# Performance work log

Hardware: AMD Instinct MI355X
Metric: run time of the kernel (lower is better)

The kernel has to match this reference:

```python
import jax, jax.numpy as jnp
import numpy as np

B, K, D = 16384, 64, 128


def setup_inputs() -> dict:
    key = jax.random.key(0)
    kx, kc = jax.random.split(key)
    x = jax.random.normal(kx, (B, D), dtype=jnp.float32)
    centers = jax.random.uniform(kc, (K, D), dtype=jnp.float32)  # torch.rand init
    return {"x": x, "centers": centers}


def reference(x, centers):
    batch, dim = x.shape
    k = centers.shape[0]
    # pairwise squared distances, same math as sum((x - c)^2)
    diff = x[:, None, :] - centers[None, :, :]          # [B, K, D]
    dist_sq = jnp.sum(diff * diff, axis=-1)             # [B, K]
    expo = -0.5 * dist_sq
    # safe softmax over clusters (identical to max-subtracted exp/sum)
    resp = jax.nn.softmax(expo, axis=-1)                # [B, K]
    log_resp = jnp.log(jnp.clip(resp, 1e-8))
    # hard assignment and per-cluster statistics
    assign = jnp.argmin(dist_sq, axis=-1)               # [B] int
    onehot = jax.nn.one_hot(assign, k, dtype=x.dtype)   # [B, K]
    cluster_weight = jnp.sum(onehot, axis=0)            # [K]
    emp_total = jnp.einsum('nk,nd->kd', onehot, x)      # [K, D]
    emp_mean = emp_total / (cluster_weight[:, None] + 1e-7)
    # masked centered samples: onehot[n,k]*(x_n - mean_k) is nonzero only at k=assign(n)
    xm = x - emp_mean[assign]                           # [B, D]
    covar_total = jnp.einsum('nk,nd,ne->kde', onehot, xm, xm)  # [K, D, D]
    covar = covar_total / (cluster_weight[:, None, None] + 1e-7)
    eye = jnp.eye(dim, dtype=x.dtype)
    covar_diag = covar * eye
    covar_off = covar * (1.0 - eye)
    diag_dist_sq = jnp.sum((covar_diag - eye) ** 2, axis=(1, 2))  # [K]
    off_dist_sq = jnp.sum(covar_off ** 2, axis=(1, 2))            # [K]
    mean_dist_sq = jnp.sum((emp_mean - centers) ** 2, axis=1)     # [K]
    mean_mse = jnp.sum(cluster_weight * mean_dist_sq) / (batch * dim)
    covar_mse = jnp.sum(
        cluster_weight * diag_dist_sq / (batch * dim)
        + cluster_weight * off_dist_sq / (batch * dim * (dim - 1.0))
    )
    return log_resp, mean_mse, covar_mse
```

## Files before the change

kernel.cpp:

```cpp
#include <hip/hip_runtime.h>

#define BB 16384
#define KK 64
#define DD 128
#define SEG 256
#define MAXITEMS 128
#define RSLAB 4096
#define RBLKS 256

typedef __attribute__((ext_vector_type(8))) short bf16x8;
typedef __attribute__((ext_vector_type(4))) float f32x4;

__device__ __forceinline__ unsigned int packbf2(float a, float b) {
    unsigned ua = __float_as_uint(a);
    unsigned ub = __float_as_uint(b);
    ua = (ua + 0x7FFFu + ((ua >> 16) & 1u)) >> 16;
    ub = (ub + 0x7FFFu + ((ub >> 16) & 1u)) >> 16;
    return ua | (ub << 16);
}

__global__ __launch_bounds__(256) void k_rows(
    const float* __restrict__ x, const float* __restrict__ centers,
    float* __restrict__ log_resp, int* __restrict__ assign,
    int* __restrict__ bhist, int* __restrict__ counter)
{
    __shared__ float xs[64][132];
    __shared__ float ct[DD][66];
    __shared__ float cn2[KK];
    __shared__ int   lh[KK];

    const int tid = threadIdx.x;
    const int row0 = blockIdx.x * 64;

    if (blockIdx.x == 0 && tid == 0) *counter = 0;
    if (tid < KK) lh[tid] = 0;

    for (int g = tid; g < 64 * 32; g += 256) {
        int r = g >> 5, c4 = g & 31;
        float4 v = ((const float4*)(x + (size_t)(row0 + r) * DD))[c4];
        *(float4*)&xs[r][c4 * 4] = v;
    }
    for (int g = tid; g < KK * 32; g += 256) {
        int k = g >> 5, c4 = g & 31;
        float4 v = ((const float4*)(centers + (size_t)k * DD))[c4];
        ct[c4 * 4 + 0][k] = v.x;
        ct[c4 * 4 + 1][k] = v.y;
        ct[c4 * 4 + 2][k] = v.z;
        ct[c4 * 4 + 3][k] = v.w;
    }
    __syncthreads();
    if (tid < KK) {
        float s = 0.f;
        for (int d = 0; d < DD; ++d) { float c = ct[d][tid]; s = fmaf(c, c, s); }
        cn2[tid] = s;
    }
    __syncthreads();

    const int tr = tid >> 5;
    const int tc = tid & 31;
    const int k0 = tc * 2, k1 = k0 + 1;

    float acc0[8], acc1[8];
    #pragma unroll
    for (int i = 0; i < 8; ++i) { acc0[i] = 0.f; acc1[i] = 0.f; }

    for (int d = 0; d < DD; d += 4) {
        float2 b0 = *(const float2*)&ct[d + 0][k0];
        float2 b1 = *(const float2*)&ct[d + 1][k0];
        float2 b2 = *(const float2*)&ct[d + 2][k0];
        float2 b3 = *(const float2*)&ct[d + 3][k0];
        #pragma unroll
        for (int i = 0; i < 8; ++i) {
            float4 a = *(const float4*)&xs[tr * 8 + i][d];
            acc0[i] = fmaf(a.x, b0.x, acc0[i]);
            acc1[i] = fmaf(a.x, b0.y, acc1[i]);
            acc0[i] = fmaf(a.y, b1.x, acc0[i]);
            acc1[i] = fmaf(a.y, b1.y, acc1[i]);
            acc0[i] = fmaf(a.z, b2.x, acc0[i]);
            acc1[i] = fmaf(a.z, b2.y, acc1[i]);
            acc0[i] = fmaf(a.w, b3.x, acc0[i]);
            acc1[i] = fmaf(a.w, b3.y, acc1[i]);
        }
    }

    const float cn0 = 0.5f * cn2[k0], cn1 = 0.5f * cn2[k1];
    #pragma unroll
    for (int i = 0; i < 8; ++i) {
        int row = row0 + tr * 8 + i;
        float v0 = acc0[i] - cn0;
        float v1 = acc1[i] - cn1;
        float m; int idx;
        if (v1 > v0) { m = v1; idx = k1; } else { m = v0; idx = k0; }
        #pragma unroll
        for (int off = 1; off < 32; off <<= 1) {
            float ov = __shfl_xor(m, off);
            int   oi = __shfl_xor(idx, off);
            if (ov > m || (ov == m && oi < idx)) { m = ov; idx = oi; }
        }
        float s = expf(v0 - m) + expf(v1 - m);
        #pragma unroll
        for (int off = 1; off < 32; off <<= 1) s += __shfl_xor(s, off);
        float ls = logf(s);
        float lr0 = fmaxf(v0 - m - ls, -18.4206807f);
        float lr1 = fmaxf(v1 - m - ls, -18.4206807f);
        *(float2*)&log_resp[(size_t)row * KK + k0] = make_float2(lr0, lr1);
        if (tc == 0) {
            assign[row] = idx;
            atomicAdd(&lh[idx], 1);
        }
    }
    __syncthreads();
    if (tid < KK) bhist[blockIdx.x * KK + tid] = lh[tid];
}

__global__ __launch_bounds__(256) void k_seg2(
    const float* __restrict__ x, const int* __restrict__ assign,
    const int* __restrict__ bhist,
    float* __restrict__ part, float* __restrict__ emp_part)
{
    __shared__ int ph_tot[4][KK];
    __shared__ int cnt_s[KK];
    __shared__ int sc[2][256];
    __shared__ int pre_s[257];
    __shared__ int myk_s, myseg_s;
    __shared__ int rows_s[SEG];
    __shared__ unsigned int XT[DD][68];

    const int tid = threadIdx.x;
    const int b = blockIdx.x;
    const int w = tid >> 6, lane = tid & 63;

    {
        const int t = tid & 63, q = tid >> 6;
        int tot = 0;
        for (int bb = q * 64; bb < q * 64 + 64; ++bb)
            tot += bhist[bb * KK + t];
        ph_tot[q][t] = tot;
    }
    __syncthreads();
    if (tid < KK)
        cnt_s[tid] = ph_tot[0][tid] + ph_tot[1][tid] + ph_tot[2][tid] + ph_tot[3][tid];
    __syncthreads();
    if (tid == 0) {
        int ic = 0;
        myk_s = -1;
        for (int k = 0; k < KK; ++k) {
            int ns = (cnt_s[k] + SEG - 1) / SEG;
            if (b >= ic && b < ic + ns) { myk_s = k; myseg_s = b - ic; }
            ic += ns;
        }
    }
    __syncthreads();
    if (myk_s < 0) return;

    const int kC = myk_s;
    const int lo = myseg_s * SEG;
    const int hi = min(lo + SEG, cnt_s[kC]);
    const int len = hi - lo;

    {
        int v = bhist[tid * KK + kC];
        sc[0][tid] = v;
        __syncthreads();
        int buf = 0;
        #pragma unroll
        for (int off = 1; off < 256; off <<= 1) {
            int nv = sc[buf][tid];
            if (tid >= off) nv += sc[buf][tid - off];
            sc[buf ^ 1][tid] = nv;
            buf ^= 1;
            __syncthreads();
        }
        if (tid == 0) pre_s[0] = 0;
        pre_s[tid + 1] = sc[buf][tid];
    }
    __syncthreads();

    for (int g = w; g < 256; g += 4) {
        int p0 = pre_s[g], p1 = pre_s[g + 1];
        if (p1 <= lo || p0 >= hi) continue;
        int a = assign[g * 64 + lane];
        bool m = (a == kC);
        unsigned long long bal = __ballot(m);
        if (m) {
            int rank = __popcll(bal & ((1ull << lane) - 1ull));
            int pos = p0 + rank;
            if (pos >= lo && pos < hi) rows_s[pos - lo] = g * 64 + lane;
        }
    }
    __syncthreads();

    const int c4 = lane & 15, q = lane >> 4;
    f32x4 acc[2][8];
    #pragma unroll
    for (int h = 0; h < 2; ++h)
        #pragma unroll
        for (int nt = 0; nt < 8; ++nt)
            acc[h][nt] = (f32x4){0.f, 0.f, 0.f, 0.f};
    float colsum = 0.f;

    for (int half = 0; half < 2; ++half) {
        const int hoff = half * 128;
        const int hlen = min(128, len - hoff);
        if (hlen <= 0) break;

        __syncthreads();
        {
            const int r0 = 2 * lane, r1 = 2 * lane + 1;
            const int d0 = w * 32;
            const float* p0 = x + (size_t)rows_s[hoff + (r0 < hlen ? r0 : 0)] * DD + d0;
            const float* p1 = x + (size_t)rows_s[hoff + (r1 < hlen ? r1 : 0)] * DD + d0;
            #pragma unroll
            for (int i = 0; i < 8; ++i) {
                float4 a = make_float4(0.f, 0.f, 0.f, 0.f);
                float4 bb = make_float4(0.f, 0.f, 0.f, 0.f);
                if (r0 < hlen) a  = *(const float4*)(p0 + 4 * i);
                if (r1 < hlen) bb = *(const float4*)(p1 + 4 * i);
                XT[d0 + 4 * i + 0][lane] = packbf2(a.x, bb.x);
                XT[d0 + 4 * i + 1][lane] = packbf2(a.y, bb.y);
                XT[d0 + 4 * i + 2][lane] = packbf2(a.z, bb.z);
                XT[d0 + 4 * i + 3][lane] = packbf2(a.w, bb.w);
            }
        }
        __syncthreads();

        if (tid < DD) {
            float s = 0.f;
            #pragma unroll
            for (int j4 = 0; j4 < 16; ++j4) {
                uint4 v = *(const uint4*)&XT[tid][j4 * 4];
                s += __uint_as_float(v.x << 16) + __uint_as_float(v.x & 0xFFFF0000u);
                s += __uint_as_float(v.y << 16) + __uint_as_float(v.y & 0xFFFF0000u);
                s += __uint_as_float(v.z << 16) + __uint_as_float(v.z & 0xFFFF0000u);
                s += __uint_as_float(v.w << 16) + __uint_as_float(v.w & 0xFFFF0000u);
            }
            colsum += s;
        }

        #pragma unroll
        for (int c = 0; c < 4; ++c) {
            const int ku = c * 16 + q * 4;
            bf16x8 a0 = *(const bf16x8*)&XT[(2 * w + 0) * 16 + c4][ku];
            bf16x8 a1 = *(const bf16x8*)&XT[(2 * w + 1) * 16 + c4][ku];
            #pragma unroll
            for (int nt = 0; nt < 8; ++nt) {
                bf16x8 bb = *(const bf16x8*)&XT[nt * 16 + c4][ku];
                acc[0][nt] = __builtin_amdgcn_mfma_f32_16x16x32_bf16(a0, bb, acc[0][nt], 0, 0, 0);
                acc[1][nt] = __builtin_amdgcn_mfma_f32_16x16x32_bf16(a1, bb, acc[1][nt], 0, 0, 0);
            }
        }
    }

    if (tid < DD) emp_part[b * DD + tid] = colsum;

    float* pb = part + (size_t)b * (DD * DD);
    #pragma unroll
    for (int h = 0; h < 2; ++h) {
        const int m0 = (2 * w + h) * 16 + q * 4;
        #pragma unroll
        for (int nt = 0; nt < 8; ++nt) {
            const int n = nt * 16 + c4;
            pb[(m0 + 0) * DD + n] = acc[h][nt].x;
            pb[(m0 + 1) * DD + n] = acc[h][nt].y;
            pb[(m0 + 2) * DD + n] = acc[h][nt].z;
            pb[(m0 + 3) * DD + n] = acc[h][nt].w;
        }
    }
}

__global__ __launch_bounds__(256) void k_redfinal(
    const float* __restrict__ part, const float* __restrict__ emp_part,
    const int* __restrict__ bhist, const float* __restrict__ centers,
    float2* __restrict__ spart, int* __restrict__ counter,
    float* __restrict__ outscalars)
{
    __shared__ int ph_tot[4][KK];
    __shared__ int cnt_s[KK], ist_s[KK], ien_s[KK];
    __shared__ float mu_s[DD], emp_s[DD];
    __shared__ float emp2[2][DD];
    __shared__ float red[4][RSLAB];

    const int tid = threadIdx.x;
    const int b = blockIdx.x;
    const int kD = b >> 2, p = b & 3;
    const int w = tid >> 6, lane = tid & 63;

    {
        const int t = tid & 63, q = tid >> 6;
        int tot = 0;
        for (int bb = q * 64; bb < q * 64 + 64; ++bb)
            tot += bhist[bb * KK + t];
        ph_tot[q][t] = tot;
    }
    __syncthreads();
    if (tid < KK)
        cnt_s[tid] = ph_tot[0][tid] + ph_tot[1][tid] + ph_tot[2][tid] + ph_tot[3][tid];
    __syncthreads();
    if (tid == 0) {
        int ic = 0;
        for (int k = 0; k < KK; ++k) {
            ist_s[k] = ic;
            ic += (cnt_s[k] + SEG - 1) / SEG;
            ien_s[k] = ic;
        }
    }
    __syncthreads();

    const int i0 = ist_s[kD], i1 = ien_s[kD];
    const float wgt = (float)cnt_s[kD];
    const float inv = 1.0f / (wgt + 1e-7f);

    {
        const int dh = tid & 127, hf = tid >> 7;
        float e0 = 0.f, e1 = 0.f;
        int it = i0 + hf;
        for (; it + 2 < i1; it += 4) {
            e0 += emp_part[it * DD + dh];
            e1 += emp_part[(it + 2) * DD + dh];
        }
        if (it < i1) e0 += emp_part[it * DD + dh];
        emp2[hf][dh] = e0 + e1;
    }
    __syncthreads();
    if (tid < DD) {
        float e = emp2[0][tid] + emp2[1][tid];
        emp_s[tid] = e;
        mu_s[tid] = e * inv;
    }

    float4 acc[16];
    #pragma unroll
    for (int c = 0; c < 16; ++c) acc[c] = make_float4(0.f, 0.f, 0.f, 0.f);

    const int base = p * RSLAB;
    for (int it = i0 + w; it < i1; it += 4) {
        const float* pb = part + (size_t)it * (DD * DD) + base;
        #pragma unroll
        for (int c = 0; c < 16; ++c) {
            float4 v = *(const float4*)&pb[c * 256 + lane * 4];
            acc[c].x += v.x; acc[c].y += v.y; acc[c].z += v.z; acc[c].w += v.w;
        }
    }
    #pragma unroll
    for (int c = 0; c < 16; ++c)
        *(float4*)&red[w][c * 256 + lane * 4] = acc[c];
    __syncthreads();

    float ds = 0.f, os = 0.f, mm = 0.f;
    #pragma unroll
    for (int jj = 0; jj < 16; ++jj) {
        int el = jj * 256 + tid;
        float sx = red[0][el] + red[1][el] + red[2][el] + red[3][el];
        int gel = base + el;
        int d = gel >> 7, e = gel & 127;
        float ctv = sx - mu_s[d] * emp_s[e] - emp_s[d] * mu_s[e]
                  + wgt * mu_s[d] * mu_s[e];
        float v = ctv * inv;
        if (d == e) { float t = v - 1.f; ds += t * t; }
        else        { os += v * v; }
    }
    if (p == 0 && tid < DD) {
        float t = mu_s[tid] - centers[kD * DD + tid];
        mm = t * t;
    }

    #pragma unroll
    for (int off = 32; off > 0; off >>= 1) {
        ds += __shfl_down(ds, off);
        os += __shfl_down(os, off);
        mm += __shfl_down(mm, off);
    }
    __shared__ float rds[4], ros[4], rmm[4];
    __shared__ int is_last;
    if (lane == 0) { rds[w] = ds; ros[w] = os; rmm[w] = mm; }
    __syncthreads();
    if (tid == 0) {
        float DS = rds[0] + rds[1] + rds[2] + rds[3];
        float OS = ros[0] + ros[1] + ros[2] + ros[3];
        float MM = rmm[0] + rmm[1] + rmm[2] + rmm[3];
        const float bd = (float)BB * (float)DD;
        float2 mine;
        mine.x = wgt * MM / bd;
        mine.y = wgt * DS / bd + wgt * OS / (bd * (float)(DD - 1));
        spart[b] = mine;
        __threadfence();
        int old = atomicAdd(counter, 1);
        is_last = (old == RBLKS - 1);
    }
    __syncthreads();
    if (is_last) {
        __threadfence();
        float2 v = spart[tid];
        float a = v.x, bb = v.y;
        #pragma unroll
        for (int off = 32; off > 0; off >>= 1) {
            a  += __shfl_down(a, off);
            bb += __shfl_down(bb, off);
        }
        __shared__ float ra[4], rb[4];
        if (lane == 0) { ra[w] = a; rb[w] = bb; }
        __syncthreads();
        if (tid == 0) {
            outscalars[0] = ra[0] + ra[1] + ra[2] + ra[3];
            outscalars[1] = rb[0] + rb[1] + rb[2] + rb[3];
        }
    }
}

extern "C" void kernel_launch(void* const* d_in, const int* in_sizes, int n_in,
                              void* d_out, int out_size, void* d_ws, size_t ws_size,
                              hipStream_t stream) {
    const float* x = (const float*)d_in[0];
    const float* centers = (const float*)d_in[1];
    float* out = (float*)d_out;
    float* outscalars = out + (size_t)BB * KK;

    char* ws = (char*)d_ws;
    size_t off = 0;
    float*  part     = (float*)(ws + off); off += (size_t)MAXITEMS * DD * DD * 4;
    float*  emp_part = (float*)(ws + off); off += MAXITEMS * DD * 4;
    int*    assign   = (int*)  (ws + off); off += BB * 4;
    int*    bhist    = (int*)  (ws + off); off += 256 * KK * 4;
    float2* spart    = (float2*)(ws + off); off += RBLKS * 8;
    int*    counter  = (int*)  (ws + off); off += 256;

    k_rows    <<<256, 256, 0, stream>>>(x, centers, out, assign, bhist, counter);
    k_seg2    <<<MAXITEMS, 256, 0, stream>>>(x, assign, bhist, part, emp_part);
    k_redfinal<<<RBLKS, 256, 0, stream>>>(part, emp_part, bhist, centers,
                                          spart, counter, outscalars);
}
```

Before: 135.3 us.

## Shrink covariance segments to 64 rows and transpose block histogram layout

```diff
diff --git a/kernel.cpp b/kernel.cpp
--- a/kernel.cpp
+++ b/kernel.cpp
@@ -3,8 +3,9 @@
 #define BB 16384
 #define KK 64
 #define DD 128
-#define SEG 256
-#define MAXITEMS 128
+#define GRP 64
+#define NGRP 256
+#define MAXITEMS 320
 #define RSLAB 4096
 #define RBLKS 256
 
@@ -22,7 +23,7 @@
 __global__ __launch_bounds__(256) void k_rows(
     const float* __restrict__ x, const float* __restrict__ centers,
     float* __restrict__ log_resp, int* __restrict__ assign,
-    int* __restrict__ bhist, int* __restrict__ counter)
+    int* __restrict__ bhistT, int* __restrict__ counter)
 {
     __shared__ float xs[64][132];
     __shared__ float ct[DD][66];
@@ -110,12 +111,12 @@
         }
     }
     __syncthreads();
-    if (tid < KK) bhist[blockIdx.x * KK + tid] = lh[tid];
+    if (tid < KK) bhistT[tid * NGRP + blockIdx.x] = lh[tid];
 }
 
 __global__ __launch_bounds__(256) void k_seg2(
     const float* __restrict__ x, const int* __restrict__ assign,
-    const int* __restrict__ bhist,
+    const int* __restrict__ bhistT,
     float* __restrict__ part, float* __restrict__ emp_part)
 {
     __shared__ int ph_tot[4][KK];
@@ -123,19 +124,23 @@
     __shared__ int sc[2][256];
     __shared__ int pre_s[257];
     __shared__ int myk_s, myseg_s;
-    __shared__ int rows_s[SEG];
-    __shared__ unsigned int XT[DD][68];
+    __shared__ int rows_s[GRP];
+    __shared__ unsigned int XR[GRP][68];
+    __shared__ unsigned int XT[DD][36];
 
     const int tid = threadIdx.x;
     const int b = blockIdx.x;
     const int w = tid >> 6, lane = tid & 63;
 
     {
-        const int t = tid & 63, q = tid >> 6;
-        int tot = 0;
-        for (int bb = q * 64; bb < q * 64 + 64; ++bb)
-            tot += bhist[bb * KK + t];
-        ph_tot[q][t] = tot;
+        const int k = tid & 63, q = tid >> 6;
+        const int* p = bhistT + k * NGRP + q * 64;
+        int t0 = 0, t1 = 0, t2 = 0, t3 = 0;
+        #pragma unroll 4
+        for (int i = 0; i < 64; i += 4) {
+            t0 += p[i]; t1 += p[i + 1]; t2 += p[i + 2]; t3 += p[i + 3];
+        }
+        ph_tot[q][k] = t0 + t1 + t2 + t3;
     }
     __syncthreads();
     if (tid < KK)
@@ -145,7 +150,7 @@
         int ic = 0;
         myk_s = -1;
         for (int k = 0; k < KK; ++k) {
-            int ns = (cnt_s[k] + SEG - 1) / SEG;
+            int ns = (cnt_s[k] + GRP - 1) / GRP;
             if (b >= ic && b < ic + ns) { myk_s = k; myseg_s = b - ic; }
             ic += ns;
         }
@@ -154,12 +159,12 @@
     if (myk_s < 0) return;
 
     const int kC = myk_s;
-    const int lo = myseg_s * SEG;
-    const int hi = min(lo + SEG, cnt_s[kC]);
+    const int lo = myseg_s * GRP;
+    const int hi = min(lo + GRP, cnt_s[kC]);
     const int len = hi - lo;
 
     {
-        int v = bhist[tid * KK + kC];
+        int v = bhistT[kC * NGRP + tid];
         sc[0][tid] = v;
         __syncthreads();
         int buf = 0;
@@ -176,7 +181,7 @@
     }
     __syncthreads();
 
-    for (int g = w; g < 256; g += 4) {
+    for (int g = w; g < NGRP; g += 4) {
         int p0 = pre_s[g], p1 = pre_s[g + 1];
         if (p1 <= lo || p0 >= hi) continue;
         int a = assign[g * 64 + lane];
@@ -190,6 +195,57 @@
     }
     __syncthreads();
 
+    #pragma unroll
+    for (int sub = 0; sub < 4; ++sub) {
+        const int j = sub * 16 + (tid >> 4);
+        const int c8 = (tid & 15) * 8;
+        float4 a = make_float4(0.f, 0.f, 0.f, 0.f);
+        float4 c = make_float4(0.f, 0.f, 0.f, 0.f);
+        if (j < len) {
+            const float* p = x + (size_t)rows_s[j] * DD + c8;
+            a = *(const float4*)p;
+            c = *(const float4*)(p + 4);
+        }
+        uint4 pk;
+        pk.x = packbf2(a.x, a.y);
+        pk.y = packbf2(a.z, a.w);
+        pk.z = packbf2(c.x, c.y);
+        pk.w = packbf2(c.z, c.w);
+        *(uint4*)&XR[j][c8 >> 1] = pk;
+    }
+    __syncthreads();
+
+    {
+        const int rp = lane & 31;
+        const int d0 = w * 32 + (lane >> 5) * 16;
+        const int dp0 = d0 >> 1;
+        uint4 a0 = *(const uint4*)&XR[2 * rp][dp0];
+        uint4 a1 = *(const uint4*)&XR[2 * rp][dp0 + 4];
+        uint4 b0 = *(const uint4*)&XR[2 * rp + 1][dp0];
+        uint4 b1 = *(const uint4*)&XR[2 * rp + 1][dp0 + 4];
+        unsigned int A[8] = {a0.x, a0.y, a0.z, a0.w, a1.x, a1.y, a1.z, a1.w};
+        unsigned int B[8] = {b0.x, b0.y, b0.z, b0.w, b1.x, b1.y, b1.z, b1.w};
+        #pragma unroll
+        for (int i = 0; i < 8; ++i) {
+            XT[d0 + 2 * i + 0][rp] = (A[i] & 0xFFFFu) | (B[i] << 16);
+            XT[d0 + 2 * i + 1][rp] = (A[i] >> 16) | (B[i] & 0xFFFF0000u);
+        }
+    }
+    __syncthreads();
+
+    if (tid < DD) {
+        float s = 0.f;
+        #pragma unroll
+        for (int j4 = 0; j4 < 8; ++j4) {
+            uint4 v = *(const uint4*)&XT[tid][j4 * 4];
+            s += __uint_as_float(v.x << 16) + __uint_as_float(v.x & 0xFFFF0000u);
+            s += __uint_as_float(v.y << 16) + __uint_as_float(v.y & 0xFFFF0000u);
+            s += __uint_as_float(v.z << 16) + __uint_as_float(v.z & 0xFFFF0000u);
+            s += __uint_as_float(v.w << 16) + __uint_as_float(v.w & 0xFFFF0000u);
+        }
+        emp_part[b * DD + tid] = s;
+    }
+
     const int c4 = lane & 15, q = lane >> 4;
     f32x4 acc[2][8];
     #pragma unroll
@@ -197,61 +253,19 @@
         #pragma unroll
         for (int nt = 0; nt < 8; ++nt)
             acc[h][nt] = (f32x4){0.f, 0.f, 0.f, 0.f};
-    float colsum = 0.f;
-
-    for (int half = 0; half < 2; ++half) {
-        const int hoff = half * 128;
-        const int hlen = min(128, len - hoff);
-        if (hlen <= 0) break;
-
-        __syncthreads();
-        {
-            const int r0 = 2 * lane, r1 = 2 * lane + 1;
-            const int d0 = w * 32;
-            const float* p0 = x + (size_t)rows_s[hoff + (r0 < hlen ? r0 : 0)] * DD + d0;
-            const float* p1 = x + (size_t)rows_s[hoff + (r1 < hlen ? r1 : 0)] * DD + d0;
-            #pragma unroll
-            for (int i = 0; i < 8; ++i) {
-                float4 a = make_float4(0.f, 0.f, 0.f, 0.f);
-                float4 bb = make_float4(0.f, 0.f, 0.f, 0.f);
-                if (r0 < hlen) a  = *(const float4*)(p0 + 4 * i);
-                if (r1 < hlen) bb = *(const float4*)(p1 + 4 * i);
-                XT[d0 + 4 * i + 0][lane] = packbf2(a.x, bb.x);
-                XT[d0 + 4 * i + 1][lane] = packbf2(a.y, bb.y);
-                XT[d0 + 4 * i + 2][lane] = packbf2(a.z, bb.z);
-                XT[d0 + 4 * i + 3][lane] = packbf2(a.w, bb.w);
-            }
-        }
-        __syncthreads();
-
-        if (tid < DD) {
-            float s = 0.f;
-            #pragma unroll
-            for (int j4 = 0; j4 < 16; ++j4) {
-                uint4 v = *(const uint4*)&XT[tid][j4 * 4];
-                s += __uint_as_float(v.x << 16) + __uint_as_float(v.x & 0xFFFF0000u);
-                s += __uint_as_float(v.y << 16) + __uint_as_float(v.y & 0xFFFF0000u);
-                s += __uint_as_float(v.z << 16) + __uint_as_float(v.z & 0xFFFF0000u);
-                s += __uint_as_float(v.w << 16) + __uint_as_float(v.w & 0xFFFF0000u);
-            }
-            colsum += s;
-        }
-
-        #pragma unroll
-        for (int c = 0; c < 4; ++c) {
-            const int ku = c * 16 + q * 4;
-            bf16x8 a0 = *(const bf16x8*)&XT[(2 * w + 0) * 16 + c4][ku];
-            bf16x8 a1 = *(const bf16x8*)&XT[(2 * w + 1) * 16 + c4][ku];
-            #pragma unroll
-            for (int nt = 0; nt < 8; ++nt) {
-                bf16x8 bb = *(const bf16x8*)&XT[nt * 16 + c4][ku];
-                acc[0][nt] = __builtin_amdgcn_mfma_f32_16x16x32_bf16(a0, bb, acc[0][nt], 0, 0, 0);
-                acc[1][nt] = __builtin_amdgcn_mfma_f32_16x16x32_bf16(a1, bb, acc[1][nt], 0, 0, 0);
-            }
-        }
-    }
-
-    if (tid < DD) emp_part[b * DD + tid] = colsum;
+
+    #pragma unroll
+    for (int c = 0; c < 2; ++c) {
+        const int ku = c * 16 + q * 4;
+        bf16x8 a0 = *(const bf16x8*)&XT[(2 * w + 0) * 16 + c4][ku];
+        bf16x8 a1 = *(const bf16x8*)&XT[(2 * w + 1) * 16 + c4][ku];
+        #pragma unroll
+        for (int nt = 0; nt < 8; ++nt) {
+            bf16x8 bb = *(const bf16x8*)&XT[nt * 16 + c4][ku];
+            acc[0][nt] = __builtin_amdgcn_mfma_f32_16x16x32_bf16(a0, bb, acc[0][nt], 0, 0, 0);
+            acc[1][nt] = __builtin_amdgcn_mfma_f32_16x16x32_bf16(a1, bb, acc[1][nt], 0, 0, 0);
+        }
+    }
 
     float* pb = part + (size_t)b * (DD * DD);
     #pragma unroll
@@ -270,7 +284,7 @@
 
 __global__ __launch_bounds__(256) void k_redfinal(
     const float* __restrict__ part, const float* __restrict__ emp_part,
-    const int* __restrict__ bhist, const float* __restrict__ centers,
+    const int* __restrict__ bhistT, const float* __restrict__ centers,
     float2* __restrict__ spart, int* __restrict__ counter,
     float* __restrict__ outscalars)
 {
@@ -286,11 +300,14 @@
     const int w = tid >> 6, lane = tid & 63;
 
     {
-        const int t = tid & 63, q = tid >> 6;
-        int tot = 0;
-        for (int bb = q * 64; bb < q * 64 + 64; ++bb)
-            tot += bhist[bb * KK + t];
-        ph_tot[q][t] = tot;
+        const int k = tid & 63, q = tid >> 6;
+        const int* pp = bhistT + k * NGRP + q * 64;
+        int t0 = 0, t1 = 0, t2 = 0, t3 = 0;
+        #pragma unroll 4
+        for (int i = 0; i < 64; i += 4) {
+            t0 += pp[i]; t1 += pp[i + 1]; t2 += pp[i + 2]; t3 += pp[i + 3];
+        }
+        ph_tot[q][k] = t0 + t1 + t2 + t3;
     }
     __syncthreads();
     if (tid < KK)
@@ -300,7 +317,7 @@
         int ic = 0;
         for (int k = 0; k < KK; ++k) {
             ist_s[k] = ic;
-            ic += (cnt_s[k] + SEG - 1) / SEG;
+            ic += (cnt_s[k] + GRP - 1) / GRP;
             ien_s[k] = ic;
         }
     }
@@ -420,12 +437,12 @@
     float*  part     = (float*)(ws + off); off += (size_t)MAXITEMS * DD * DD * 4;
     float*  emp_part = (float*)(ws + off); off += MAXITEMS * DD * 4;
     int*    assign   = (int*)  (ws + off); off += BB * 4;
-    int*    bhist    = (int*)  (ws + off); off += 256 * KK * 4;
+    int*    bhistT   = (int*)  (ws + off); off += KK * NGRP * 4;
     float2* spart    = (float2*)(ws + off); off += RBLKS * 8;
     int*    counter  = (int*)  (ws + off); off += 256;
 
-    k_rows    <<<256, 256, 0, stream>>>(x, centers, out, assign, bhist, counter);
-    k_seg2    <<<MAXITEMS, 256, 0, stream>>>(x, assign, bhist, part, emp_part);
-    k_redfinal<<<RBLKS, 256, 0, stream>>>(part, emp_part, bhist, centers,
+    k_rows    <<<256, 256, 0, stream>>>(x, centers, out, assign, bhistT, counter);
+    k_seg2    <<<MAXITEMS, 256, 0, stream>>>(x, assign, bhistT, part, emp_part);
+    k_redfinal<<<RBLKS, 256, 0, stream>>>(part, emp_part, bhistT, centers,
                                           spart, counter, outscalars);
 }
```

Result: faster. 131.6 us (-2.7%).
